# Kernel tuning notes

Hardware: AMD Instinct MI355X
Metric: run time of the kernel (lower is better)

## Reference

```python
import jax, jax.numpy as jnp
import numpy as np

N = 12288
E = 393216
D_IN, D_HID, D_OUT = 128, 128, 64


def gcn_conv(x, edge_index, W, b, num_nodes):
    # PyG GCNConv: h = x @ W; add self-loops; sym-normalize; scatter-add; + b
    h = x @ W  # [N, F]
    row, col = edge_index[0], edge_index[1]
    sl = jnp.arange(num_nodes, dtype=edge_index.dtype)
    row = jnp.concatenate([row, sl])
    col = jnp.concatenate([col, sl])
    deg = jax.ops.segment_sum(jnp.ones_like(col, dtype=h.dtype), col, num_segments=num_nodes)
    dinv = jax.lax.rsqrt(jnp.maximum(deg, 1e-12))
    norm = dinv[row] * dinv[col]  # [E+N]
    msgs = h[row] * norm[:, None]
    out = jax.ops.segment_sum(msgs, col, num_segments=num_nodes)
    return out + b


def setup_inputs() -> dict:
    key = jax.random.key(0)
    k1, k2, k3, k4, k5 = jax.random.split(key, 5)
    x = jax.random.uniform(k1, (N, D_IN), dtype=jnp.float32)
    edge_index = jax.random.randint(k2, (2, E), 0, N, dtype=jnp.int64)
    # Glorot-style init for GCN weights, zeros for biases (PyG defaults)
    W1 = jax.random.normal(k3, (D_IN, D_HID), dtype=jnp.float32) * (1.0 / np.sqrt(D_IN))
    b1 = jnp.zeros((D_HID,), dtype=jnp.float32)
    W2 = jax.random.normal(k4, (D_HID, D_OUT), dtype=jnp.float32) * (1.0 / np.sqrt(D_HID))
    b2 = jnp.zeros((D_OUT,), dtype=jnp.float32)
    return {"x": x, "edge_index": edge_index, "W1": W1, "b1": b1, "W2": W2, "b2": b2}


def reference(x, edge_index, W1, b1, W2, b2):
    h = jax.nn.relu(gcn_conv(x, edge_index, W1, b1, N))
    latent = gcn_conv(h, edge_index, W2, b2, N)  # [N, D_OUT]
    return latent @ latent.T  # [N, N] gram-matrix decoder
```

## Files before the change

kernel.cpp:

```cpp
#include <hip/hip_runtime.h>

#define NN   12288
#define EE   393216
#define DIN  128
#define DHID 128
#define DOUT 64
#define CAP  96

typedef __attribute__((ext_vector_type(8))) short bf16x8;
typedef __attribute__((ext_vector_type(4))) float f32x4;

__device__ __forceinline__ short f2bf(float f) {
    unsigned u = __float_as_uint(f);
    unsigned r = (u + 0x7fffu + ((u >> 16) & 1u)) >> 16;
    return (short)r;
}
__device__ __forceinline__ float bf2f(short h) {
    return __uint_as_float(((unsigned)(unsigned short)h) << 16);
}

#define GEMM1_BLOCKS 768
#define FILL_BLOCKS  256
__global__ __launch_bounds__(256) void k_fill_gemm1(const float* __restrict__ x,
                                                    const int* __restrict__ row,
                                                    const int* __restrict__ col,
                                                    const float* __restrict__ W1,
                                                    unsigned* __restrict__ cursor,
                                                    int* __restrict__ bucket,
                                                    float* __restrict__ g1) {
    const int b = blockIdx.x, t = threadIdx.x;
    if (b < GEMM1_BLOCKS) {
        __shared__ float xs[16 * DIN];
        const int r0 = b * 16;
        for (int j = t; j < 16 * DIN; j += 256) xs[j] = x[(size_t)r0 * DIN + j];
        __syncthreads();
        const int c = t & 127, rg = (t >> 7) * 8;
        float acc[8] = {};
        for (int k = 0; k < DIN; ++k) {
            float w = W1[k * DHID + c];
#pragma unroll
            for (int r = 0; r < 8; ++r) acc[r] += xs[(rg + r) * DIN + k] * w;
        }
#pragma unroll
        for (int r = 0; r < 8; ++r) g1[(size_t)(r0 + rg + r) * DHID + c] = acc[r];
    } else {
        const int gid = (b - GEMM1_BLOCKS) * 256 + t;
        for (int e = gid; e < EE; e += FILL_BLOCKS * 256) {
            int c = col[e];
            unsigned p = atomicAdd(&cursor[c], 1u);
            if (p < CAP) bucket[(size_t)c * CAP + p] = row[e];
        }
    }
}

__global__ __launch_bounds__(256) void k_gather1(const float* __restrict__ g1,
                                                 const int* __restrict__ bucket,
                                                 const unsigned* __restrict__ cursor,
                                                 const float* __restrict__ b1,
                                                 float* __restrict__ hrelu) {
    const int lane = threadIdx.x & 63, wave = threadIdx.x >> 6;
    const int c = blockIdx.x * 4 + wave;
    const unsigned cnt = cursor[c];
    const float dc = rsqrtf((float)cnt + 1.0f);
    const unsigned e = cnt < CAP ? cnt : CAP;
    const float2* __restrict__ G = (const float2*)g1;
    const int* __restrict__ bk = bucket + (size_t)c * CAP;
    float2 a = G[(size_t)c * 64 + lane];
    float accx = a.x * dc, accy = a.y * dc;
    unsigned i = 0;
    for (; i + 4 <= e; i += 4) {
        int r0 = bk[i], r1 = bk[i + 1], r2 = bk[i + 2], r3 = bk[i + 3];
        float d0 = rsqrtf((float)cursor[r0] + 1.0f);
        float d1 = rsqrtf((float)cursor[r1] + 1.0f);
        float d2 = rsqrtf((float)cursor[r2] + 1.0f);
        float d3 = rsqrtf((float)cursor[r3] + 1.0f);
        float2 v0 = G[(size_t)r0 * 64 + lane];
        float2 v1 = G[(size_t)r1 * 64 + lane];
        float2 v2 = G[(size_t)r2 * 64 + lane];
        float2 v3 = G[(size_t)r3 * 64 + lane];
        accx += (v0.x * d0 + v1.x * d1) + (v2.x * d2 + v3.x * d3);
        accy += (v0.y * d0 + v1.y * d1) + (v2.y * d2 + v3.y * d3);
    }
    for (; i < e; ++i) {
        int r = bk[i];
        float d = rsqrtf((float)cursor[r] + 1.0f);
        float2 v = G[(size_t)r * 64 + lane];
        accx += v.x * d;
        accy += v.y * d;
    }
    float2 bb = ((const float2*)b1)[lane];
    float ox = accx * dc + bb.x;
    float oy = accy * dc + bb.y;
    float2 o;
    o.x = ox > 0.f ? ox : 0.f;
    o.y = oy > 0.f ? oy : 0.f;
    ((float2*)hrelu)[(size_t)c * 64 + lane] = o;
}

__global__ __launch_bounds__(256) void k_gemm2(const float* __restrict__ h,
                                               const float* __restrict__ W2,
                                               const unsigned* __restrict__ cursor,
                                               float* __restrict__ g2) {
    __shared__ float hs[16 * DHID];
    const int t = threadIdx.x;
    const int r0 = blockIdx.x * 16;
    for (int j = t; j < 16 * DHID; j += 256) hs[j] = h[(size_t)r0 * DHID + j];
    __syncthreads();
    const int c = t & 63, rg = (t >> 6) * 4;
    float acc[4] = {};
    for (int k = 0; k < DHID; ++k) {
        float w = W2[k * DOUT + c];
#pragma unroll
        for (int r = 0; r < 4; ++r) acc[r] += hs[(rg + r) * DHID + k] * w;
    }
#pragma unroll
    for (int r = 0; r < 4; ++r) {
        float d = rsqrtf((float)cursor[r0 + rg + r] + 1.0f);
        g2[(size_t)(r0 + rg + r) * DOUT + c] = acc[r] * d;
    }
}

__global__ __launch_bounds__(256) void k_gather2(const float* __restrict__ g2,
                                                 const int* __restrict__ bucket,
                                                 const unsigned* __restrict__ cursor,
                                                 const float* __restrict__ b2,
                                                 short* __restrict__ H,
                                                 short* __restrict__ Lo) {
    const int lane = threadIdx.x & 63, wave = threadIdx.x >> 6;
    const int c = blockIdx.x * 4 + wave;
    const unsigned cnt = cursor[c];
    const float dc = rsqrtf((float)cnt + 1.0f);
    const unsigned e = cnt < CAP ? cnt : CAP;
    const int* __restrict__ bk = bucket + (size_t)c * CAP;
    float acc = g2[(size_t)c * DOUT + lane];
    unsigned i = 0;
    for (; i + 4 <= e; i += 4) {
        int r0 = bk[i], r1 = bk[i + 1], r2 = bk[i + 2], r3 = bk[i + 3];
        float v0 = g2[(size_t)r0 * DOUT + lane];
        float v1 = g2[(size_t)r1 * DOUT + lane];
        float v2 = g2[(size_t)r2 * DOUT + lane];
        float v3 = g2[(size_t)r3 * DOUT + lane];
        acc += (v0 + v1) + (v2 + v3);
    }
    for (; i < e; ++i) acc += g2[(size_t)bk[i] * DOUT + lane];
    float v = acc * dc + b2[lane];
    short h = f2bf(v);
    H[(size_t)c * DOUT + lane] = h;
    Lo[(size_t)c * DOUT + lane] = f2bf(v - bf2f(h));
}

#define NTILE 96
#define NPAIR ((NTILE * (NTILE + 1)) / 2)
__global__ __launch_bounds__(256) void k_gram(const short* __restrict__ H,
                                              const short* __restrict__ L,
                                              float* __restrict__ out) {
    __shared__ float T[4][64][65];
    const int tid  = threadIdx.x;
    const int lane = tid & 63;
    const int wave = tid >> 6;

    const int Lb = blockIdx.x;
    int bi = (int)((193.0f - sqrtf(193.0f * 193.0f - 8.0f * (float)Lb)) * 0.5f);
    if (bi < 0) bi = 0;
    if (bi > NTILE - 1) bi = NTILE - 1;
    while (bi * NTILE - (bi * (bi - 1)) / 2 > Lb) --bi;
    while ((bi + 1) * NTILE - ((bi + 1) * bi) / 2 <= Lb) ++bi;
    const int bj = bi + (Lb - (bi * NTILE - (bi * (bi - 1)) / 2));

    const int wm = wave >> 1, wn = wave & 1;
    const int row0 = bi * 128 + wm * 64;
    const int col0 = bj * 128 + wn * 64;
    const int fr = lane & 15;
    const int fk = (lane >> 4) << 3;
    const int crow = (lane >> 4) * 4;
    const bool mirror = (bi != bj);

    bf16x8 aH[4][2], aL[4][2];
#pragma unroll
    for (int m = 0; m < 4; ++m)
#pragma unroll
        for (int k = 0; k < 2; ++k) {
            size_t off = (size_t)(row0 + m * 16 + fr) * DOUT + k * 32 + fk;
            aH[m][k] = *(const bf16x8*)(H + off);
            aL[m][k] = *(const bf16x8*)(L + off);
        }

#pragma unroll
    for (int n = 0; n < 4; ++n) {
        bf16x8 bH[2], bL[2];
#pragma unroll
        for (int k = 0; k < 2; ++k) {
            size_t off = (size_t)(col0 + n * 16 + fr) * DOUT + k * 32 + fk;
            bH[k] = *(const bf16x8*)(H + off);
            bL[k] = *(const bf16x8*)(L + off);
        }
        f32x4 acc[4];
#pragma unroll
        for (int m = 0; m < 4; ++m) acc[m] = (f32x4){0.f, 0.f, 0.f, 0.f};

#pragma unroll
        for (int m = 0; m < 4; ++m)
#pragma unroll
            for (int k = 0; k < 2; ++k) {
                acc[m] = __builtin_amdgcn_mfma_f32_16x16x32_bf16(aL[m][k], bH[k], acc[m], 0, 0, 0);
                acc[m] = __builtin_amdgcn_mfma_f32_16x16x32_bf16(aH[m][k], bL[k], acc[m], 0, 0, 0);
                acc[m] = __builtin_amdgcn_mfma_f32_16x16x32_bf16(aH[m][k], bH[k], acc[m], 0, 0, 0);
            }

#pragma unroll
        for (int m = 0; m < 4; ++m) {
            size_t base = (size_t)(row0 + m * 16 + crow) * NN + col0 + n * 16 + fr;
#pragma unroll
            for (int j = 0; j < 4; ++j)
                __builtin_nontemporal_store(acc[m][j], &out[base + (size_t)j * NN]);
        }
        if (mirror) {
#pragma unroll
            for (int m = 0; m < 4; ++m)
#pragma unroll
                for (int j = 0; j < 4; ++j)
                    T[wave][n * 16 + fr][m * 16 + crow + j] = acc[m][j];
        }
    }

    if (mirror) {
#pragma unroll
        for (int rr = 0; rr < 16; ++rr) {
            int lrow = rr * 4 + (lane >> 4);
            int c4 = (lane & 15) * 4;
            f32x4 v;
            v.x = T[wave][lrow][c4 + 0];
            v.y = T[wave][lrow][c4 + 1];
            v.z = T[wave][lrow][c4 + 2];
            v.w = T[wave][lrow][c4 + 3];
            __builtin_nontemporal_store(v, (f32x4*)&out[(size_t)(col0 + lrow) * NN + row0 + c4]);
        }
    }
}

extern "C" void kernel_launch(void* const* d_in, const int* in_sizes, int n_in,
                              void* d_out, int out_size, void* d_ws, size_t ws_size,
                              hipStream_t stream) {
    const float* x  = (const float*)d_in[0];
    const int*   ei = (const int*)d_in[1];
    const float* W1 = (const float*)d_in[2];
    const float* b1 = (const float*)d_in[3];
    const float* W2 = (const float*)d_in[4];
    const float* b2 = (const float*)d_in[5];
    float* out = (float*)d_out;

    const int* row = ei;
    const int* col = ei + EE;

    char* w = (char*)d_ws;
    unsigned* cursor = (unsigned*)w; w += (size_t)NN * 4;
    int*      bucket = (int*)w;      w += (size_t)NN * CAP * 4;
    float*    g1     = (float*)w;    w += (size_t)NN * DHID * 4;
    float*    hrelu  = (float*)w;    w += (size_t)NN * DHID * 4;
    float*    g2     = (float*)w;    w += (size_t)NN * DOUT * 4;
    short*    latH   = (short*)w;    w += (size_t)NN * DOUT * 2;
    short*    latL   = (short*)w;    w += (size_t)NN * DOUT * 2;

    hipMemsetAsync(cursor, 0, (size_t)NN * 4, stream);

    k_fill_gemm1<<<GEMM1_BLOCKS + FILL_BLOCKS, 256, 0, stream>>>(x, row, col, W1, cursor, bucket, g1);
    k_gather1<<<NN / 4, 256, 0, stream>>>(g1, bucket, cursor, b1, hrelu);
    k_gemm2<<<NN / 16, 256, 0, stream>>>(hrelu, W2, cursor, g2);
    k_gather2<<<NN / 4, 256, 0, stream>>>(g2, bucket, cursor, b2, latH, latL);

    k_gram<<<NPAIR, 256, 0, stream>>>(latH, latL, out);
}
```

Baseline: 244.6 us.

## Fuse layer-1 gather with layer-2 GEMM and stage gram tile in shared memory

Merges the first aggregation kernel with the second GEMM: each wave keeps its ReLU'd row in shared memory and computes the 64-wide projection directly, removing the hrelu round trip and one launch. Separately, the gram kernel now writes the full 128x128 tile into a padded shared buffer and emits fully coalesced 512-byte row stores for both the tile and its mirror, instead of scattered per-lane stores. This costs a larger shared allocation (about 66KB), which may reduce occupancy, plus an extra block barrier. The fused GEMM reads W2 from global per wave with no reuse across rows.

Result: faster. 220.4 us (-9.9%).

```diff
diff --git a/kernel.cpp b/kernel.cpp
--- a/kernel.cpp
+++ b/kernel.cpp
@@ -53,11 +53,13 @@
     }
 }
 
-__global__ __launch_bounds__(256) void k_gather1(const float* __restrict__ g1,
-                                                 const int* __restrict__ bucket,
-                                                 const unsigned* __restrict__ cursor,
-                                                 const float* __restrict__ b1,
-                                                 float* __restrict__ hrelu) {
+__global__ __launch_bounds__(256) void k_gather1_gemm2(const float* __restrict__ g1,
+                                                       const int* __restrict__ bucket,
+                                                       const unsigned* __restrict__ cursor,
+                                                       const float* __restrict__ b1,
+                                                       const float* __restrict__ W2,
+                                                       float* __restrict__ g2) {
+    __shared__ float hs[4][DHID];
     const int lane = threadIdx.x & 63, wave = threadIdx.x >> 6;
     const int c = blockIdx.x * 4 + wave;
     const unsigned cnt = cursor[c];
@@ -94,30 +96,12 @@
     float2 o;
     o.x = ox > 0.f ? ox : 0.f;
     o.y = oy > 0.f ? oy : 0.f;
-    ((float2*)hrelu)[(size_t)c * 64 + lane] = o;
-}
-
-__global__ __launch_bounds__(256) void k_gemm2(const float* __restrict__ h,
-                                               const float* __restrict__ W2,
-                                               const unsigned* __restrict__ cursor,
-                                               float* __restrict__ g2) {
-    __shared__ float hs[16 * DHID];
-    const int t = threadIdx.x;
-    const int r0 = blockIdx.x * 16;
-    for (int j = t; j < 16 * DHID; j += 256) hs[j] = h[(size_t)r0 * DHID + j];
+    ((float2*)hs[wave])[lane] = o;
     __syncthreads();
-    const int c = t & 63, rg = (t >> 6) * 4;
-    float acc[4] = {};
-    for (int k = 0; k < DHID; ++k) {
-        float w = W2[k * DOUT + c];
-#pragma unroll
-        for (int r = 0; r < 4; ++r) acc[r] += hs[(rg + r) * DHID + k] * w;
-    }
-#pragma unroll
-    for (int r = 0; r < 4; ++r) {
-        float d = rsqrtf((float)cursor[r0 + rg + r] + 1.0f);
-        g2[(size_t)(r0 + rg + r) * DOUT + c] = acc[r] * d;
-    }
+    float acc = 0.f;
+#pragma unroll 8
+    for (int k = 0; k < DHID; ++k) acc += hs[wave][k] * W2[k * DOUT + lane];
+    g2[(size_t)c * DOUT + lane] = acc * dc;
 }
 
 __global__ __launch_bounds__(256) void k_gather2(const float* __restrict__ g2,
@@ -154,7 +138,7 @@
 __global__ __launch_bounds__(256) void k_gram(const short* __restrict__ H,
                                               const short* __restrict__ L,
                                               float* __restrict__ out) {
-    __shared__ float T[4][64][65];
+    __shared__ float P[128][132];
     const int tid  = threadIdx.x;
     const int lane = tid & 63;
     const int wave = tid >> 6;
@@ -208,32 +192,32 @@
             }
 
 #pragma unroll
-        for (int m = 0; m < 4; ++m) {
-            size_t base = (size_t)(row0 + m * 16 + crow) * NN + col0 + n * 16 + fr;
+        for (int m = 0; m < 4; ++m)
 #pragma unroll
             for (int j = 0; j < 4; ++j)
-                __builtin_nontemporal_store(acc[m][j], &out[base + (size_t)j * NN]);
-        }
-        if (mirror) {
-#pragma unroll
-            for (int m = 0; m < 4; ++m)
-#pragma unroll
-                for (int j = 0; j < 4; ++j)
-                    T[wave][n * 16 + fr][m * 16 + crow + j] = acc[m][j];
-        }
-    }
-
+                P[wm * 64 + m * 16 + crow + j][wn * 64 + n * 16 + fr] = acc[m][j];
+    }
+    __syncthreads();
+
+    const size_t gr0 = (size_t)bi * 128, gc0 = (size_t)bj * 128;
+#pragma unroll
+    for (int it = 0; it < 16; ++it) {
+        int idx = it * 256 + tid;
+        int r = idx >> 5, c4 = (idx & 31) << 2;
+        f32x4 v = *(const f32x4*)&P[r][c4];
+        __builtin_nontemporal_store(v, (f32x4*)&out[(gr0 + r) * NN + gc0 + c4]);
+    }
     if (mirror) {
 #pragma unroll
-        for (int rr = 0; rr < 16; ++rr) {
-            int lrow = rr * 4 + (lane >> 4);
-            int c4 = (lane & 15) * 4;
+        for (int it = 0; it < 16; ++it) {
+            int idx = it * 256 + tid;
+            int r = idx >> 5, c4 = (idx & 31) << 2;
             f32x4 v;
-            v.x = T[wave][lrow][c4 + 0];
-            v.y = T[wave][lrow][c4 + 1];
-            v.z = T[wave][lrow][c4 + 2];
-            v.w = T[wave][lrow][c4 + 3];
-            __builtin_nontemporal_store(v, (f32x4*)&out[(size_t)(col0 + lrow) * NN + row0 + c4]);
+            v.x = P[c4 + 0][r];
+            v.y = P[c4 + 1][r];
+            v.z = P[c4 + 2][r];
+            v.w = P[c4 + 3][r];
+            __builtin_nontemporal_store(v, (f32x4*)&out[(gc0 + r) * NN + gr0 + c4]);
         }
     }
 }
@@ -256,7 +240,6 @@
     unsigned* cursor = (unsigned*)w; w += (size_t)NN * 4;
     int*      bucket = (int*)w;      w += (size_t)NN * CAP * 4;
     float*    g1     = (float*)w;    w += (size_t)NN * DHID * 4;
-    float*    hrelu  = (float*)w;    w += (size_t)NN * DHID * 4;
     float*    g2     = (float*)w;    w += (size_t)NN * DOUT * 4;
     short*    latH   = (short*)w;    w += (size_t)NN * DOUT * 2;
     short*    latL   = (short*)w;    w += (size_t)NN * DOUT * 2;
@@ -264,8 +247,7 @@
     hipMemsetAsync(cursor, 0, (size_t)NN * 4, stream);
 
     k_fill_gemm1<<<GEMM1_BLOCKS + FILL_BLOCKS, 256, 0, stream>>>(x, row, col, W1, cursor, bucket, g1);
-    k_gather1<<<NN / 4, 256, 0, stream>>>(g1, bucket, cursor, b1, hrelu);
-    k_gemm2<<<NN / 16, 256, 0, stream>>>(hrelu, W2, cursor, g2);
+    k_gather1_gemm2<<<NN / 4, 256, 0, stream>>>(g1, bucket, cursor, b1, W2, g2);
     k_gather2<<<NN / 4, 256, 0, stream>>>(g2, bucket, cursor, b2, latH, latL);
 
     k_gram<<<NPAIR, 256, 0, stream>>>(latH, latL, out);
```
